# Kernel tuning notes

Hardware: AMD Instinct MI355X
Metric: run time of the kernel (lower is better)

The kernel has to match this reference:

```python
import jax, jax.numpy as jnp
import numpy as np
from jax import lax

B, T = 8, 256
GRID = (8, 8, 8)
X, Y, Z = GRID
N = X * Y * Z            # 512 nodes
C_IN = C_OUT = 8         # 4096 / 512
R = 8                    # num_rand


def _stencil_mask():
    # 7-point stencil mask at kernel center (1,1,1)
    m = np.zeros((3, 3, 3), dtype=np.float32)
    c = 1
    m[c, c, c] = 1.0
    m[c - 1, c, c] = 1.0
    m[c + 1, c, c] = 1.0
    m[c, c - 1, c] = 1.0
    m[c, c + 1, c] = 1.0
    m[c, c, c - 1] = 1.0
    m[c, c, c + 1] = 1.0
    return jnp.asarray(m)


def setup_inputs() -> dict:
    key = jax.random.key(0)
    k1, k2, k3, k4 = jax.random.split(key, 4)
    x = jax.random.normal(k1, (B, T, C_IN * N), dtype=jnp.float32)
    # MaskedConv3d params (kernel 3x3x3)
    fan = C_IN * 27
    conv_w = jax.random.normal(k2, (C_OUT, C_IN, 3, 3, 3), dtype=jnp.float32) / np.sqrt(fan)
    conv_b = jnp.zeros((C_OUT,), dtype=jnp.float32)
    # RandomGraphMixer3D params (xavier-uniform-like)
    bound = np.sqrt(6.0 / (C_IN * R + C_OUT))
    mix_w = jax.random.uniform(k3, (C_OUT, C_IN, R), jnp.float32, -bound, bound)
    mix_b = jnp.zeros((C_OUT,), dtype=jnp.float32)
    rand_indices = jax.random.randint(k4, (N, R), 0, N, dtype=jnp.int32)
    alpha = jnp.float32(0.5)
    return {"x": x, "conv_w": conv_w, "conv_b": conv_b,
            "mix_w": mix_w, "mix_b": mix_b, "alpha": alpha,
            "rand_indices": rand_indices}


def reference(x, conv_w, conv_b, mix_w, mix_b, alpha, rand_indices):
    Bd, Td, D = x.shape
    xt = x.reshape(Bd * Td, C_IN, X, Y, Z)
    # --- masked 7-point stencil conv3d ---
    w = conv_w * _stencil_mask()  # broadcast over (O, I)
    y_local = lax.conv_general_dilated(
        xt, w, window_strides=(1, 1, 1), padding='SAME',
        dimension_numbers=('NCDHW', 'OIDHW', 'NCDHW'))
    y_local = y_local + conv_b[None, :, None, None, None]
    # --- random graph mixer: gather + contract ---
    x_nodes = xt.reshape(Bd * Td, C_IN, N)
    gathered = x_nodes[:, :, rand_indices]              # [BT, C, N, R]
    y_rand = jnp.einsum('ocr,bcnr->bon', mix_w, gathered) + mix_b[None, :, None]
    y_rand = y_rand.reshape(Bd * Td, C_OUT, X, Y, Z)
    # --- sigmoid blend ---
    a = jax.nn.sigmoid(alpha)
    yt = a * y_local + (1.0 - a) * y_rand
    return yt.reshape(Bd, Td, C_OUT * N)
```

## Files before the change

### kernel.cpp

```cpp
#include <hip/hip_runtime.h>
#include <math.h>

#define NNODES 512
#define CIN 8
#define COUT 8
#define RR 8
#define BTB 4
#define GUARD 64
#define CH_STRIDE 656
#define SLAB_HW (CIN * CH_STRIDE)
#define LDS_HW (BTB * SLAB_HW)

typedef __attribute__((ext_vector_type(8))) short short8;
typedef __attribute__((ext_vector_type(4))) float floatx4;

__global__ void prep_weights(const float* __restrict__ conv_w,
                             const float* __restrict__ conv_b,
                             const float* __restrict__ mix_w,
                             const float* __restrict__ mix_b,
                             const float* __restrict__ alpha_p,
                             float* __restrict__ ws) {
    const int t = threadIdx.x;
    const float alpha = alpha_p[0];
    const float a = 1.0f / (1.0f + expf(-alpha));
    if (t < 960) {
        const int oc = t / 15;
        const int tap = t % 15;
        float v;
        if (tap < 7) {
            const int off[7] = {13, 4, 22, 10, 16, 12, 14};
            v = a * conv_w[oc * 27 + off[tap]];
        } else {
            v = (1.0f - a) * mix_w[oc * RR + (tap - 7)];
        }
        ws[t] = v;
    } else if (t < 968) {
        const int o = t - 960;
        ws[960 + o] = a * conv_b[o] + (1.0f - a) * mix_b[o];
    }
}

__device__ __forceinline__ unsigned int bf16_rne(float a) {
    unsigned int u = __float_as_uint(a);
    return (u + 0x7fffu + ((u >> 16) & 1u)) >> 16;
}
__device__ __forceinline__ unsigned int pack_bf16(float a, float b) {
    unsigned int ua = __float_as_uint(a);
    unsigned int ub = __float_as_uint(b);
    ua = (ua + 0x7fffu + ((ua >> 16) & 1u)) >> 16;
    ub = (ub + 0x7fffu + ((ub >> 16) & 1u)) & 0xffff0000u;
    return ua | ub;
}

__global__ __launch_bounds__(256) void hybrid3d_mfma(
    const float* __restrict__ x,
    const int*   __restrict__ rand_idx,
    const float* __restrict__ wsb,
    float* __restrict__ out)
{
    __shared__ unsigned short lds16[LDS_HW];

    const int tid  = threadIdx.x;
    const int wave = tid >> 6;
    const int lane = tid & 63;
    const int quad = lane >> 4;
    const int r16  = lane & 15;
    const int oddh = quad & 1;
    const int c0   = quad >> 1;

    {
        uint4* z = (uint4*)lds16;
#pragma unroll
        for (int i = 0; i < 11; ++i) {
            const int idx = tid + i * 256;
            if (idx < LDS_HW / 8) z[idx] = make_uint4(0u, 0u, 0u, 0u);
        }
    }

    short8 bfrag[4];
#pragma unroll
    for (int ch = 0; ch < 4; ++ch) {
        union { unsigned int u[4]; short8 s; } bf;
#pragma unroll
        for (int jp = 0; jp < 4; ++jp) {
            const int gk = ch * 32 + quad * 8 + 2 * jp;
            const int c  = gk >> 4;
            const int tap = gk & 15;
            float f0 = (r16 < 8 && tap < 15)     ? wsb[(r16 * CIN + c) * 15 + tap]     : 0.0f;
            float f1 = (r16 < 8 && tap + 1 < 15) ? wsb[(r16 * CIN + c) * 15 + tap + 1] : 0.0f;
            bf.u[jp] = pack_bf16(f0, f1);
        }
        bfrag[ch] = bf.s;
    }
    const float bias = (r16 < 8) ? wsb[960 + r16] : 0.0f;

    __syncthreads();

    {
        const float* xg = x + (size_t)blockIdx.x * (BTB * CIN * NNODES);
#pragma unroll
        for (int k = 0; k < 8; ++k) {
            const int q    = tid + k * 256;
            const int bt_l = q >> 9;
            const int rem  = q & 511;
            const int c    = rem >> 6;
            const int m0   = (rem & 63) << 3;
            const float4* src = (const float4*)(xg + bt_l * (CIN * NNODES) + c * NNODES + m0);
            float4 f0 = src[0], f1 = src[1];
            uint4 pk;
            pk.x = pack_bf16(f0.x, f0.y);
            pk.y = pack_bf16(f0.z, f0.w);
            pk.z = pack_bf16(f1.x, f1.y);
            pk.w = pack_bf16(f1.z, f1.w);
            *((uint4*)&lds16[bt_l * SLAB_HW + c * CH_STRIDE + GUARD + m0]) = pk;
        }
    }
    __syncthreads();

    const int db = wave * SLAB_HW + c0 * CH_STRIDE + GUARD;
    float* outb = out + ((size_t)blockIdx.x * BTB + wave) * (COUT * NNODES);

    for (int t = 0; t < 32; ++t) {
        const int m = t * 16 + r16;
        const int h = (m >> 3) & 7;
        const int w = m & 7;

        const int4* ip = (const int4*)(rand_idx + m * RR);
        const int4 i0 = ip[0];
        const int4 i1 = ip[1];

        const int sb = db + m;
        int va[8];
        va[0] = oddh ? (db + i0.y) : sb;
        va[1] = oddh ? (db + i0.z) : sb - 64;
        va[2] = oddh ? (db + i0.w) : sb + 64;
        va[3] = oddh ? (db + i1.x) : sb - 8;
        va[4] = oddh ? (db + i1.y) : sb + 8;
        va[5] = oddh ? (db + i1.z) : sb - 1;
        va[6] = oddh ? (db + i1.w) : sb + 1;
        va[7] = oddh ? sb          : (db + i0.x);

        const bool ok3 = oddh || (h > 0);
        const bool ok4 = oddh || (h < 7);
        const bool ok5 = oddh || (w > 0);
        const bool ok6 = oddh || (w < 7);
        const bool ok7 = !oddh;

        floatx4 acc = {bias, bias, bias, bias};

#pragma unroll
        for (int ch = 0; ch < 4; ++ch) {
            const int off = ch * 2 * CH_STRIDE;
            unsigned int v0 = lds16[va[0] + off];
            unsigned int v1 = lds16[va[1] + off];
            unsigned int v2 = lds16[va[2] + off];
            unsigned int v3 = lds16[va[3] + off];
            unsigned int v4 = lds16[va[4] + off];
            unsigned int v5 = lds16[va[5] + off];
            unsigned int v6 = lds16[va[6] + off];
            unsigned int v7 = lds16[va[7] + off];
            v3 = ok3 ? v3 : 0u;
            v4 = ok4 ? v4 : 0u;
            v5 = ok5 ? v5 : 0u;
            v6 = ok6 ? v6 : 0u;
            v7 = ok7 ? v7 : 0u;
            union { unsigned int u[4]; short8 s; } af;
            af.u[0] = v0 | (v1 << 16);
            af.u[1] = v2 | (v3 << 16);
            af.u[2] = v4 | (v5 << 16);
            af.u[3] = v6 | (v7 << 16);
            acc = __builtin_amdgcn_mfma_f32_16x16x32_bf16(af.s, bfrag[ch], acc, 0, 0, 0);
        }

        if (r16 < 8) {
            float4* dst = (float4*)(outb + r16 * NNODES + t * 16 + quad * 4);
            *dst = *(float4*)&acc;
        }
    }
}

extern "C" void kernel_launch(void* const* d_in, const int* in_sizes, int n_in,
                              void* d_out, int out_size, void* d_ws, size_t ws_size,
                              hipStream_t stream) {
    const float* x       = (const float*)d_in[0];
    const float* conv_w  = (const float*)d_in[1];
    const float* conv_b  = (const float*)d_in[2];
    const float* mix_w   = (const float*)d_in[3];
    const float* mix_b   = (const float*)d_in[4];
    const float* alpha_p = (const float*)d_in[5];
    const int*   rand_i  = (const int*)d_in[6];
    float* out = (float*)d_out;
    float* ws  = (float*)d_ws;

    const int BT = in_sizes[0] / (CIN * NNODES);

    prep_weights<<<1, 1024, 0, stream>>>(conv_w, conv_b, mix_w, mix_b, alpha_p, ws);
    hybrid3d_mfma<<<BT / BTB, 256, 0, stream>>>(x, rand_i, ws, out);
}
```

Baseline: 116.6 us.

## Switch LDS to node-major channel-packed layout with precomputed tap offset table

The shared-memory layout changes from channel-major to node-major, with all 8 bf16 channels of a node packed into one 16-byte slot. Each MFMA A-fragment becomes a single 128-bit LDS load instead of eight scalar 16-bit loads plus masking and packing. A prep kernel builds a per-lane table of byte offsets for the stencil and random taps, with out-of-bounds taps pointing at a zero guard slot. This removes the per-iteration index arithmetic and the rand_idx loads. Two independent accumulators break the MFMA dependency chain, and each wave loads its own slab; the trade-offs are extra global table reads and uncoalesced-ish strided x loads.

```diff
diff --git a/kernel.cpp b/kernel.cpp
--- a/kernel.cpp
+++ b/kernel.cpp
@@ -7,22 +7,31 @@
 #define RR 8
 #define BTB 4
 #define GUARD 64
-#define CH_STRIDE 656
-#define SLAB_HW (CIN * CH_STRIDE)
+#define SLOTS (GUARD + NNODES + GUARD)
+#define SLAB_HW (SLOTS * 8)
 #define LDS_HW (BTB * SLAB_HW)
+#define WTAB 1024
 
 typedef __attribute__((ext_vector_type(8))) short short8;
 typedef __attribute__((ext_vector_type(4))) float floatx4;
 
-__global__ void prep_weights(const float* __restrict__ conv_w,
-                             const float* __restrict__ conv_b,
-                             const float* __restrict__ mix_w,
-                             const float* __restrict__ mix_b,
-                             const float* __restrict__ alpha_p,
-                             float* __restrict__ ws) {
+__device__ __forceinline__ unsigned int pack_bf16(float a, float b) {
+    unsigned int ua = __float_as_uint(a);
+    unsigned int ub = __float_as_uint(b);
+    ua = (ua + 0x7fffu + ((ua >> 16) & 1u)) >> 16;
+    ub = (ub + 0x7fffu + ((ub >> 16) & 1u)) & 0xffff0000u;
+    return ua | ub;
+}
+
+__global__ void prep(const float* __restrict__ conv_w,
+                     const float* __restrict__ conv_b,
+                     const float* __restrict__ mix_w,
+                     const float* __restrict__ mix_b,
+                     const float* __restrict__ alpha_p,
+                     const int*   __restrict__ rand_idx,
+                     float* __restrict__ ws) {
     const int t = threadIdx.x;
-    const float alpha = alpha_p[0];
-    const float a = 1.0f / (1.0f + expf(-alpha));
+    const float a = 1.0f / (1.0f + expf(-alpha_p[0]));
     if (t < 960) {
         const int oc = t / 15;
         const int tap = t % 15;
@@ -38,143 +47,115 @@
         const int o = t - 960;
         ws[960 + o] = a * conv_b[o] + (1.0f - a) * mix_b[o];
     }
+
+    int4* tab = (int4*)((int*)ws + WTAB);
+    for (int e = t; e < 2048; e += 1024) {
+        const int tt = e >> 6, lane = e & 63;
+        const int q = lane >> 4, r16 = lane & 15;
+        const int m = tt * 16 + r16;
+        const int h = (m >> 3) & 7, w = m & 7;
+        int off[4];
+#pragma unroll
+        for (int i = 0; i < 4; ++i) {
+            const int tap = 4 * i + q;
+            int o;
+            if (tap == 0)       o = GUARD + m;
+            else if (tap == 1)  o = GUARD + m - 64;
+            else if (tap == 2)  o = GUARD + m + 64;
+            else if (tap == 3)  o = (h > 0) ? (GUARD + m - 8) : 0;
+            else if (tap == 4)  o = (h < 7) ? (GUARD + m + 8) : 0;
+            else if (tap == 5)  o = (w > 0) ? (GUARD + m - 1) : 0;
+            else if (tap == 6)  o = (w < 7) ? (GUARD + m + 1) : 0;
+            else if (tap <= 14) o = GUARD + rand_idx[m * RR + (tap - 7)];
+            else                o = 0;
+            off[i] = o * 16;
+        }
+        tab[e] = make_int4(off[0], off[1], off[2], off[3]);
+    }
 }
 
-__device__ __forceinline__ unsigned int bf16_rne(float a) {
-    unsigned int u = __float_as_uint(a);
-    return (u + 0x7fffu + ((u >> 16) & 1u)) >> 16;
-}
-__device__ __forceinline__ unsigned int pack_bf16(float a, float b) {
-    unsigned int ua = __float_as_uint(a);
-    unsigned int ub = __float_as_uint(b);
-    ua = (ua + 0x7fffu + ((ua >> 16) & 1u)) >> 16;
-    ub = (ub + 0x7fffu + ((ub >> 16) & 1u)) & 0xffff0000u;
-    return ua | ub;
-}
-
-__global__ __launch_bounds__(256) void hybrid3d_mfma(
+__global__ __launch_bounds__(256) void hybrid3d_v2(
     const float* __restrict__ x,
-    const int*   __restrict__ rand_idx,
     const float* __restrict__ wsb,
     float* __restrict__ out)
 {
     __shared__ unsigned short lds16[LDS_HW];
-
     const int tid  = threadIdx.x;
     const int wave = tid >> 6;
     const int lane = tid & 63;
     const int quad = lane >> 4;
     const int r16  = lane & 15;
-    const int oddh = quad & 1;
-    const int c0   = quad >> 1;
 
     {
-        uint4* z = (uint4*)lds16;
-#pragma unroll
-        for (int i = 0; i < 11; ++i) {
-            const int idx = tid + i * 256;
-            if (idx < LDS_HW / 8) z[idx] = make_uint4(0u, 0u, 0u, 0u);
+        const uint4 z = make_uint4(0u, 0u, 0u, 0u);
+        for (int g = tid; g < BTB * 2 * GUARD; g += 256) {
+            const int b = g >> 7;
+            const int s = g & 127;
+            const int slot = (s < GUARD) ? s : (NNODES + s);
+            *(uint4*)&lds16[b * SLAB_HW + slot * 8] = z;
         }
     }
 
     short8 bfrag[4];
 #pragma unroll
-    for (int ch = 0; ch < 4; ++ch) {
+    for (int i = 0; i < 4; ++i) {
+        const int tap = 4 * i + quad;
         union { unsigned int u[4]; short8 s; } bf;
 #pragma unroll
         for (int jp = 0; jp < 4; ++jp) {
-            const int gk = ch * 32 + quad * 8 + 2 * jp;
-            const int c  = gk >> 4;
-            const int tap = gk & 15;
-            float f0 = (r16 < 8 && tap < 15)     ? wsb[(r16 * CIN + c) * 15 + tap]     : 0.0f;
-            float f1 = (r16 < 8 && tap + 1 < 15) ? wsb[(r16 * CIN + c) * 15 + tap + 1] : 0.0f;
+            const int c0 = 2 * jp, c1 = 2 * jp + 1;
+            float f0 = (r16 < 8 && tap < 15) ? wsb[(r16 * CIN + c0) * 15 + tap] : 0.0f;
+            float f1 = (r16 < 8 && tap < 15) ? wsb[(r16 * CIN + c1) * 15 + tap] : 0.0f;
             bf.u[jp] = pack_bf16(f0, f1);
         }
-        bfrag[ch] = bf.s;
+        bfrag[i] = bf.s;
     }
     const float bias = (r16 < 8) ? wsb[960 + r16] : 0.0f;
 
-    __syncthreads();
-
-    {
-        const float* xg = x + (size_t)blockIdx.x * (BTB * CIN * NNODES);
+    const float* xg = x + ((size_t)blockIdx.x * BTB + wave) * (CIN * NNODES);
+    unsigned short* slab = lds16 + wave * SLAB_HW;
 #pragma unroll
-        for (int k = 0; k < 8; ++k) {
-            const int q    = tid + k * 256;
-            const int bt_l = q >> 9;
-            const int rem  = q & 511;
-            const int c    = rem >> 6;
-            const int m0   = (rem & 63) << 3;
-            const float4* src = (const float4*)(xg + bt_l * (CIN * NNODES) + c * NNODES + m0);
-            float4 f0 = src[0], f1 = src[1];
-            uint4 pk;
-            pk.x = pack_bf16(f0.x, f0.y);
-            pk.y = pack_bf16(f0.z, f0.w);
-            pk.z = pack_bf16(f1.x, f1.y);
-            pk.w = pack_bf16(f1.z, f1.w);
-            *((uint4*)&lds16[bt_l * SLAB_HW + c * CH_STRIDE + GUARD + m0]) = pk;
-        }
+    for (int j = 0; j < 8; ++j) {
+        const int n = lane + 64 * j;
+        float v[8];
+#pragma unroll
+        for (int c = 0; c < 8; ++c) v[c] = xg[c * NNODES + n];
+        uint4 pk;
+        pk.x = pack_bf16(v[0], v[1]);
+        pk.y = pack_bf16(v[2], v[3]);
+        pk.z = pack_bf16(v[4], v[5]);
+        pk.w = pack_bf16(v[6], v[7]);
+        *(uint4*)&slab[(GUARD + n) * 8] = pk;
     }
     __syncthreads();
 
-    const int db = wave * SLAB_HW + c0 * CH_STRIDE + GUARD;
+    const char* slabp = (const char*)slab;
+    const int4* tab = (const int4*)((const int*)wsb + WTAB);
     float* outb = out + ((size_t)blockIdx.x * BTB + wave) * (COUT * NNODES);
 
+#pragma unroll 2
     for (int t = 0; t < 32; ++t) {
-        const int m = t * 16 + r16;
-        const int h = (m >> 3) & 7;
-        const int w = m & 7;
+        const int4 off = tab[t * 64 + lane];
+        union { uint4 u; short8 s; } r0, r1, r2, r3;
+        r0.u = *(const uint4*)(slabp + off.x);
+        r1.u = *(const uint4*)(slabp + off.y);
+        r2.u = *(const uint4*)(slabp + off.z);
+        r3.u = *(const uint4*)(slabp + off.w);
 
-        const int4* ip = (const int4*)(rand_idx + m * RR);
-        const int4 i0 = ip[0];
-        const int4 i1 = ip[1];
-
-        const int sb = db + m;
-        int va[8];
-        va[0] = oddh ? (db + i0.y) : sb;
-        va[1] = oddh ? (db + i0.z) : sb - 64;
-        va[2] = oddh ? (db + i0.w) : sb + 64;
-        va[3] = oddh ? (db + i1.x) : sb - 8;
-        va[4] = oddh ? (db + i1.y) : sb + 8;
-        va[5] = oddh ? (db + i1.z) : sb - 1;
-        va[6] = oddh ? (db + i1.w) : sb + 1;
-        va[7] = oddh ? sb          : (db + i0.x);
-
-        const bool ok3 = oddh || (h > 0);
-        const bool ok4 = oddh || (h < 7);
-        const bool ok5 = oddh || (w > 0);
-        const bool ok6 = oddh || (w < 7);
-        const bool ok7 = !oddh;
-
-        floatx4 acc = {bias, bias, bias, bias};
-
-#pragma unroll
-        for (int ch = 0; ch < 4; ++ch) {
-            const int off = ch * 2 * CH_STRIDE;
-            unsigned int v0 = lds16[va[0] + off];
-            unsigned int v1 = lds16[va[1] + off];
-            unsigned int v2 = lds16[va[2] + off];
-            unsigned int v3 = lds16[va[3] + off];
-            unsigned int v4 = lds16[va[4] + off];
-            unsigned int v5 = lds16[va[5] + off];
-            unsigned int v6 = lds16[va[6] + off];
-            unsigned int v7 = lds16[va[7] + off];
-            v3 = ok3 ? v3 : 0u;
-            v4 = ok4 ? v4 : 0u;
-            v5 = ok5 ? v5 : 0u;
-            v6 = ok6 ? v6 : 0u;
-            v7 = ok7 ? v7 : 0u;
-            union { unsigned int u[4]; short8 s; } af;
-            af.u[0] = v0 | (v1 << 16);
-            af.u[1] = v2 | (v3 << 16);
-            af.u[2] = v4 | (v5 << 16);
-            af.u[3] = v6 | (v7 << 16);
-            acc = __builtin_amdgcn_mfma_f32_16x16x32_bf16(af.s, bfrag[ch], acc, 0, 0, 0);
-        }
+        floatx4 acc_a = {bias, bias, bias, bias};
+        floatx4 acc_b = {0.0f, 0.0f, 0.0f, 0.0f};
+        acc_a = __builtin_amdgcn_mfma_f32_16x16x32_bf16(r0.s, bfrag[0], acc_a, 0, 0, 0);
+        acc_b = __builtin_amdgcn_mfma_f32_16x16x32_bf16(r2.s, bfrag[2], acc_b, 0, 0, 0);
+        acc_a = __builtin_amdgcn_mfma_f32_16x16x32_bf16(r1.s, bfrag[1], acc_a, 0, 0, 0);
+        acc_b = __builtin_amdgcn_mfma_f32_16x16x32_bf16(r3.s, bfrag[3], acc_b, 0, 0, 0);
 
         if (r16 < 8) {
-            float4* dst = (float4*)(outb + r16 * NNODES + t * 16 + quad * 4);
-            *dst = *(float4*)&acc;
+            float4 res;
+            res.x = acc_a.x + acc_b.x;
+            res.y = acc_a.y + acc_b.y;
+            res.z = acc_a.z + acc_b.z;
+            res.w = acc_a.w + acc_b.w;
+            *(float4*)(outb + r16 * NNODES + t * 16 + quad * 4) = res;
         }
     }
 }
@@ -194,6 +175,6 @@
 
     const int BT = in_sizes[0] / (CIN * NNODES);
 
-    prep_weights<<<1, 1024, 0, stream>>>(conv_w, conv_b, mix_w, mix_b, alpha_p, ws);
-    hybrid3d_mfma<<<BT / BTB, 256, 0, stream>>>(x, rand_i, ws, out);
+    prep<<<1, 1024, 0, stream>>>(conv_w, conv_b, mix_w, mix_b, alpha_p, rand_i, ws);
+    hybrid3d_v2<<<BT / BTB, 256, 0, stream>>>(x, ws, out);
 }
```

New measurement: 110.2 us. -5.5%, faster.
